# Kernel tuning notes

Hardware: AMD Instinct MI355X
Metric: run time of the kernel (lower is better)

## Reference

```python
import jax, jax.numpy as jnp
import numpy as np
from functools import partial

WARMUP = 365   # init kwarg warmup_length
HYDRODT = 1.0  # daily step

# (name, lower, upper) -- stands in for MODEL_PARAM_DICT['sac']['param_range']
PARAM_RANGES = [
    ("KC", 0.1, 1.2), ("PCTIM", 0.0, 0.1), ("ADIMP", 0.0, 0.3),
    ("UZTWM", 10.0, 100.0), ("UZFWM", 10.0, 100.0), ("LZTWM", 50.0, 400.0),
    ("LZFSM", 10.0, 100.0), ("LZFPM", 50.0, 1000.0), ("RSERV", 0.0, 0.3),
    ("PFREE", 0.0, 0.5), ("RIVA", 0.0, 0.1), ("ZPERC", 5.0, 350.0),
    ("REXP", 1.0, 4.0), ("UZK", 0.1, 0.5), ("LZSK", 0.01, 0.35),
    ("LZPK", 0.001, 0.05), ("CI", 0.5, 0.9), ("CGS", 0.95, 0.998),
    ("CGP", 0.98, 0.998), ("KE", 0.0, 1.0), ("XE", 0.0, 0.5),
]
_LO = np.array([r[1] for r in PARAM_RANGES], dtype=np.float32)
_HI = np.array([r[2] for r in PARAM_RANGES], dtype=np.float32)


def _scale_params(parameters):
    ps = _LO + parameters * (_HI - _LO)  # (n_basin, 21)
    return {name: ps[:, i] for i, (name, _, _) in enumerate(PARAM_RANGES)}


def _sac_step(prm, carry, pe_t):
    (auztw, alztw, uztw, uzfw, lztw, lzfs, lzfp, qs, qi, qgs, qgp, mq) = carry
    kc, pctim, adimp = prm["KC"], prm["PCTIM"], prm["ADIMP"]
    uztwm, uzfwm, lztwm = prm["UZTWM"], prm["UZFWM"], prm["LZTWM"]
    lzfsm, lzfpm = prm["LZFSM"], prm["LZFPM"]
    pfree, riva = prm["PFREE"], prm["RIVA"]
    zperc, rexp, uzk = prm["ZPERC"], prm["REXP"], prm["UZK"]
    lzsk, lzpk = prm["LZSK"], prm["LZPK"]
    ci, cgs, cgp, ke, xe = prm["CI"], prm["CGS"], prm["CGP"], prm["KE"], prm["XE"]

    p = jnp.maximum(pe_t[:, 0], 0.0)
    e = jnp.maximum(jnp.nan_to_num(pe_t[:, 1], nan=0.0, posinf=0.0, neginf=0.0), 0.0)
    ep = kc * e
    # --- impervious / alterable-impervious area ---
    roimp = pctim * p
    ae2 = pctim * ep
    ae1 = jnp.minimum(auztw, ep * (auztw / uztwm))
    ae3 = jnp.maximum((ep - ae1) * (alztw / (uztwm + lztwm)), 0.0)
    pav = jnp.maximum(p - (uztwm - (auztw - ae1)), 0.0)
    adsur = jnp.maximum(pav * ((alztw - ae3) / lztwm), 0.0)
    ars = jnp.maximum(pav - adsur + (alztw - ae3) - lztwm, 0.0)
    auztw = jnp.maximum(jnp.minimum(uztwm, auztw - ae1 + p), 0.0)
    alztw = jnp.maximum(jnp.minimum(lztwm, pav - adsur + (alztw - ae3)), 0.0)
    # --- permeable-area evaporation ---
    e1 = jnp.minimum(uztw, ep * (uztw / uztwm))
    e2 = jnp.maximum(jnp.minimum(uzfw, ep - e1), 0.0)
    e3 = jnp.maximum((ep - e1 - e2) * (lztw / (uztwm + lztwm)), 0.0)
    lt1 = jnp.maximum(lztw - e3, 0.0)
    e4 = riva * ep
    et = ae2 + ae1 + ae3 + e1 + e2 + e3 + e4
    adsur_adimp = adsur * adimp
    ars_adimp = ars * adimp
    parea = 1.0 - pctim - adimp
    # --- permeable-area runoff ---
    rs = jnp.maximum(p + (uztw + uzfw - e1 - e2) - (uztwm + uzfwm), 0.0) * parea
    ut = jnp.maximum(jnp.minimum(uztwm, uztw - e1 + p), 0.0)
    uf = jnp.maximum(jnp.minimum(uzfwm, p + (uztw + uzfw - e1 - e2) - ut), 0.0)
    ri = uf * uzk
    uf = jnp.maximum(uf - ri, 0.0)
    # --- percolation into the lower zone ---
    pbase = lzfsm * lzsk + lzfpm * lzpk
    defr = jnp.maximum(1.0 - (lzfs + lzfp + lt1) / (lzfsm + lzfpm + lztwm), 0.0)
    perc = pbase * (1.0 + zperc * jnp.power(defr, rexp)) * uf / uzfwm
    rate = jnp.maximum(jnp.minimum(perc, (lzfsm + lzfpm + lztwm) - (lzfs + lzfp + lt1)), 0.0)
    uf = jnp.maximum(uf - rate, 0.0)
    fx = jnp.maximum(jnp.minimum(lzfsm + lzfpm - (lzfs + lzfp),
                                 jnp.maximum(rate - (lztwm - lt1), rate * pfree)), 0.0)
    perct = rate - fx
    coef = (lzfpm / (lzfsm + lzfpm)) * (2.0 * (1.0 - lzfp / lzfpm)
           / ((1.0 - lzfp / lzfpm) + (1.0 - lzfs / lzfsm)))
    coef = jnp.minimum(coef, 1.0)
    percp = jnp.maximum(jnp.minimum(lzfpm - lzfp,
                                    jnp.maximum(fx - (lzfsm - lzfs), coef * fx)), 0.0)
    percs = jnp.maximum(fx - percp, 0.0)
    lt = jnp.minimum(lt1 + perct, lztwm)
    ls = lzfs + percs
    lp = lzfp + percp
    rgs = ls * lzsk
    ls = jnp.maximum(ls - rgs, 0.0)
    rgp = lp * lzpk
    lp = jnp.maximum(lp - rgp, 0.0)
    # --- area-weighted runoff components ---
    ri_p, rgs_p, rgp_p = ri * parea, rgs * parea, rgp * parea
    rs_tot = roimp + adsur_adimp + ars_adimp + rs
    # --- slope routing: linear reservoirs ---
    i1 = qs + qi + qgs + qgp  # previous-step total channel inflow
    qs_n = rs_tot
    qi_n = ci * qi + (1.0 - ci) * ri_p
    qgs_n = cgs * qgs + (1.0 - cgs) * rgs_p
    qgp_n = cgp * qgp + (1.0 - cgp) * rgp_p
    i2 = qs_n + qi_n + qgs_n + qgp_n
    # --- river routing: Muskingum, single reach (rivernumber = 1) ---
    dt = 0.5 * HYDRODT
    denom = ke * (1.0 - xe) + dt
    c1 = (ke * xe + dt) / denom
    c2 = (dt - ke * xe) / denom
    c3 = (ke * (1.0 - xe) - dt) / denom
    o1 = mq[:, 0]
    o2 = c1 * i1 + c2 * i2 + c3 * o1
    mq_n = o2[:, None]
    carry_n = (auztw, alztw, ut, uf, lt, ls, lp, qs_n, qi_n, qgs_n, qgp_n, mq_n)
    return carry_n, (et, o2)


def _sac_run(p_and_e, parameters, step_wrap=lambda f: f):
    prm = _scale_params(parameters)
    n_basin = parameters.shape[0]
    s01 = jnp.full((n_basin,), 0.01, dtype=p_and_e.dtype)
    carry = tuple(s01 for _ in range(11)) + (jnp.full((n_basin, 1), 0.01, dtype=p_and_e.dtype),)
    step = step_wrap(partial(_sac_step, prm))
    if WARMUP > 0:
        carry, _ = jax.lax.scan(step, carry, p_and_e[:WARMUP])
        carry = jax.tree_util.tree_map(jax.lax.stop_gradient, carry)  # torch no_grad warmup
    _, (e_sim, q_sim) = jax.lax.scan(step, carry, p_and_e[WARMUP:])
    return jnp.stack([q_sim, e_sim])  # (2, n_step, n_basin)


def setup_inputs() -> dict:
    key = jax.random.key(0)
    k1, k2, k3 = jax.random.split(key, 3)
    T, B = 1825, 10000
    prcp = jax.random.uniform(k1, (T, B), minval=0.0, maxval=20.0)  # mm/day
    pet = jax.random.uniform(k3, (T, B), minval=0.0, maxval=6.0)    # mm/day
    p_and_e = jnp.stack([prcp, pet], axis=-1).astype(jnp.float32)
    parameters = jax.random.uniform(k2, (B, 21), minval=0.01, maxval=0.99).astype(jnp.float32)
    return {"p_and_e": p_and_e, "parameters": parameters}


def reference(p_and_e, parameters):
    return _sac_run(p_and_e, parameters)
```

## Files before the change

kernel.cpp:

```cpp
#include <hip/hip_runtime.h>
#include <math.h>

#define T_TOTAL 1825
#define WARMUP_T 365
#define T_OUT (T_TOTAL - WARMUP_T)
#define NB 10000

__global__ __launch_bounds__(64, 1)
void sac_kernel(const float* __restrict__ p_and_e,
                const float* __restrict__ params,
                float* __restrict__ out)
{
    const int b = blockIdx.x * blockDim.x + threadIdx.x;
    if (b >= NB) return;

    const float* pr = params + b * 21;
    const float kc    = 0.1f   + pr[0]  * (1.2f - 0.1f);
    const float pctim = 0.0f   + pr[1]  * (0.1f - 0.0f);
    const float adimp = 0.0f   + pr[2]  * (0.3f - 0.0f);
    const float uztwm = 10.0f  + pr[3]  * (100.0f - 10.0f);
    const float uzfwm = 10.0f  + pr[4]  * (100.0f - 10.0f);
    const float lztwm = 50.0f  + pr[5]  * (400.0f - 50.0f);
    const float lzfsm = 10.0f  + pr[6]  * (100.0f - 10.0f);
    const float lzfpm = 50.0f  + pr[7]  * (1000.0f - 50.0f);
    const float pfree = 0.0f   + pr[9]  * (0.5f - 0.0f);
    const float riva  = 0.0f   + pr[10] * (0.1f - 0.0f);
    const float zperc = 5.0f   + pr[11] * (350.0f - 5.0f);
    const float rexp  = 1.0f   + pr[12] * (4.0f - 1.0f);
    const float uzk   = 0.1f   + pr[13] * (0.5f - 0.1f);
    const float lzsk  = 0.01f  + pr[14] * (0.35f - 0.01f);
    const float lzpk  = 0.001f + pr[15] * (0.05f - 0.001f);
    const float ci    = 0.5f   + pr[16] * (0.9f - 0.5f);
    const float cgs   = 0.95f  + pr[17] * (0.998f - 0.95f);
    const float cgp   = 0.98f  + pr[18] * (0.998f - 0.98f);
    const float ke    = 0.0f   + pr[19] * (1.0f - 0.0f);
    const float xe    = 0.0f   + pr[20] * (0.5f - 0.0f);

    const float inv_uztwm = 1.0f / uztwm;
    const float inv_lztwm = 1.0f / lztwm;
    const float inv_uzfwm = 1.0f / uzfwm;
    const float inv_uzlz  = 1.0f / (uztwm + lztwm);
    const float uz_sum    = uztwm + uzfwm;
    const float lzall     = lzfsm + lzfpm + lztwm;
    const float inv_lzall = 1.0f / lzall;
    const float lzfsfp    = lzfsm + lzfpm;
    const float ratio_fp  = lzfpm / lzfsfp;
    const float inv_lzfpm = 1.0f / lzfpm;
    const float inv_lzfsm = 1.0f / lzfsm;
    const float pbase     = lzfsm * lzsk + lzfpm * lzpk;
    const float parea     = 1.0f - pctim - adimp;
    const float one_m_ci  = 1.0f - ci;
    const float one_m_cgs = 1.0f - cgs;
    const float one_m_cgp = 1.0f - cgp;
    const float dt    = 0.5f;
    const float denom = ke * (1.0f - xe) + dt;
    const float c1 = (ke * xe + dt) / denom;
    const float c2 = (dt - ke * xe) / denom;
    const float c3 = (ke * (1.0f - xe) - dt) / denom;

    float auztw = 0.01f, alztw = 0.01f;
    float uztw = 0.01f, uzfw = 0.01f, lztw = 0.01f;
    float lzfs = 0.01f, lzfp = 0.01f;
    float qs = 0.01f, qi = 0.01f, qgs = 0.01f, qgp = 0.01f;
    float o_prev = 0.01f;

    const float2* __restrict__ pe2 = (const float2*)p_and_e;
    float* __restrict__ q_out = out;
    float* __restrict__ e_out = out + (size_t)T_OUT * NB;

    unsigned lidx = (unsigned)b;
    unsigned sidx = (unsigned)b;

    auto step = [&](float2 pe, bool do_store) {
        const float p = fmaxf(pe.x, 0.0f);
        const float e = fmaxf(pe.y, 0.0f);

        const float ep    = kc * e;

        const float ae1   = fminf(auztw, ep * (auztw * inv_uztwm));
        const float ae3   = fmaxf((ep - ae1) * (alztw * inv_uzlz), 0.0f);
        const float pav   = fmaxf(p - (uztwm - (auztw - ae1)), 0.0f);
        const float alz3  = alztw - ae3;
        const float adsur = fmaxf(pav * (alz3 * inv_lztwm), 0.0f);
        const float ars   = fmaxf(pav - adsur + alz3 - lztwm, 0.0f);
        const float auztw_n = fmaxf(fminf(uztwm, auztw - ae1 + p), 0.0f);
        const float alztw_n = fmaxf(fminf(lztwm, pav - adsur + alz3), 0.0f);

        const float gp = 1.0f - lzfp * inv_lzfpm;
        const float gs = 1.0f - lzfs * inv_lzfsm;
        float coef = ratio_fp * (2.0f * gp) * __builtin_amdgcn_rcpf(gp + gs);
        coef = fminf(coef, 1.0f);

        const float e1  = fminf(uztw, ep * (uztw * inv_uztwm));
        const float e2  = fmaxf(fminf(uzfw, ep - e1), 0.0f);
        const float e3  = fmaxf((ep - e1 - e2) * (lztw * inv_uzlz), 0.0f);
        const float lt1 = fmaxf(lztw - e3, 0.0f);

        const float uz_avail = p + (uztw + uzfw - e1 - e2);
        const float rs = fmaxf(uz_avail - uz_sum, 0.0f) * parea;
        const float ut = fmaxf(fminf(uztwm, uztw - e1 + p), 0.0f);
        float uf = fmaxf(fminf(uzfwm, uz_avail - ut), 0.0f);
        const float ri = uf * uzk;
        uf = fmaxf(uf - ri, 0.0f);

        const float lzsum = lzfs + lzfp + lt1;
        const float defr  = fmaxf(1.0f - lzsum * inv_lzall, 0.0f);
        const float dpow  = __builtin_amdgcn_exp2f(rexp * __builtin_amdgcn_logf(defr));
        const float perc  = pbase * (1.0f + zperc * dpow) * uf * inv_uzfwm;
        const float rate  = fmaxf(fminf(perc, lzall - lzsum), 0.0f);
        uf = fmaxf(uf - rate, 0.0f);

        const float fx = fmaxf(fminf(lzfsfp - (lzfs + lzfp),
                                     fmaxf(rate - (lztwm - lt1), rate * pfree)),
                               0.0f);
        const float perct = rate - fx;
        const float percp = fmaxf(fminf(lzfpm - lzfp,
                                        fmaxf(fx - (lzfsm - lzfs), coef * fx)),
                                  0.0f);
        const float percs = fmaxf(fx - percp, 0.0f);

        const float lt = fminf(lt1 + perct, lztwm);
        float ls = lzfs + percs;
        float lp = lzfp + percp;
        const float rgs = ls * lzsk;
        ls = fmaxf(ls - rgs, 0.0f);
        const float rgp = lp * lzpk;
        lp = fmaxf(lp - rgp, 0.0f);

        const float ri_p   = ri * parea;
        const float rgs_p  = rgs * parea;
        const float rgp_p  = rgp * parea;
        const float rs_tot = (pctim * p + adsur * adimp) + (ars * adimp + rs);

        const float i1 = (qs + qi) + (qgs + qgp);
        qs  = rs_tot;
        qi  = ci  * qi  + one_m_ci  * ri_p;
        qgs = cgs * qgs + one_m_cgs * rgs_p;
        qgp = cgp * qgp + one_m_cgp * rgp_p;
        const float i2 = (qs + qi) + (qgs + qgp);
        const float o2 = c1 * i1 + c2 * i2 + c3 * o_prev;
        o_prev = o2;

        if (do_store) {
            const float ae2 = pctim * ep;
            const float e4  = riva * ep;
            const float et  = (ae2 + ae1) + (ae3 + e1) + (e2 + e3) + e4;
            q_out[sidx] = o2;
            e_out[sidx] = et;
            sidx += NB;
        }

        auztw = auztw_n; alztw = alztw_n;
        uztw = ut; uzfw = uf; lztw = lt; lzfs = ls; lzfp = lp;
    };

    float2 f0 = pe2[lidx];
    float2 f1 = pe2[lidx + 1u * NB];
    float2 f2 = pe2[lidx + 2u * NB];
    float2 f3 = pe2[lidx + 3u * NB];
    lidx += 4u * NB;

    for (int g = 0; g < 91; ++g) {
        const float2 n0 = pe2[lidx];
        const float2 n1 = pe2[lidx + 1u * NB];
        const float2 n2 = pe2[lidx + 2u * NB];
        const float2 n3 = pe2[lidx + 3u * NB];
        lidx += 4u * NB;
        step(f0, false); step(f1, false); step(f2, false); step(f3, false);
        f0 = n0; f1 = n1; f2 = n2; f3 = n3;
    }
    {
        const float2 n0 = pe2[lidx];
        lidx += NB;
        step(f0, false);
        f0 = f1; f1 = f2; f2 = f3; f3 = n0;
    }

    for (int g = 0; g < 364; ++g) {
        const float2 n0 = pe2[lidx];
        const float2 n1 = pe2[lidx + 1u * NB];
        const float2 n2 = pe2[lidx + 2u * NB];
        const float2 n3 = pe2[lidx + 3u * NB];
        lidx += 4u * NB;
        step(f0, true); step(f1, true); step(f2, true); step(f3, true);
        f0 = n0; f1 = n1; f2 = n2; f3 = n3;
    }
    step(f0, true); step(f1, true); step(f2, true); step(f3, true);
}

extern "C" void kernel_launch(void* const* d_in, const int* in_sizes, int n_in,
                              void* d_out, int out_size, void* d_ws, size_t ws_size,
                              hipStream_t stream) {
    const float* p_and_e = (const float*)d_in[0];
    const float* params  = (const float*)d_in[1];
    float* out = (float*)d_out;

    const int block = 64;
    const int grid = (NB + block - 1) / block;
    sac_kernel<<<grid, block, 0, stream>>>(p_and_e, params, out);
}
```

Measured before the change: 681.1 us.

## Process two basins per thread with paired arithmetic and vectorized loads/stores

Each thread now simulates two adjacent basins using a paired-float struct, halving the thread count. Input loads become float4 and output stores float2. The aim is to interleave two independent dependency chains for ILP and enable packed FP32 math, and to widen memory accesses. The risk is that per-thread work doubles while occupancy halves, so total latency may rise if the chains were not bubble-bound.

```diff
diff --git a/kernel.cpp b/kernel.cpp
--- a/kernel.cpp
+++ b/kernel.cpp
@@ -5,183 +5,211 @@
 #define WARMUP_T 365
 #define T_OUT (T_TOTAL - WARMUP_T)
 #define NB 10000
+#define NPAIR 5000
+
+#define DI __device__ __forceinline__
+
+struct F2 { float a, b; };
+
+DI F2 operator+(F2 x, F2 y){ return {x.a + y.a, x.b + y.b}; }
+DI F2 operator-(F2 x, F2 y){ return {x.a - y.a, x.b - y.b}; }
+DI F2 operator*(F2 x, F2 y){ return {x.a * y.a, x.b * y.b}; }
+DI F2 operator+(float x, F2 y){ return {x + y.a, x + y.b}; }
+DI F2 operator-(float x, F2 y){ return {x - y.a, x - y.b}; }
+DI F2 operator*(float x, F2 y){ return {x * y.a, x * y.b}; }
+DI F2 vmin(F2 x, F2 y){ return {fminf(x.a, y.a), fminf(x.b, y.b)}; }
+DI F2 vmin(F2 x, float y){ return {fminf(x.a, y), fminf(x.b, y)}; }
+DI F2 vmax(F2 x, F2 y){ return {fmaxf(x.a, y.a), fmaxf(x.b, y.b)}; }
+DI F2 vmax(F2 x, float y){ return {fmaxf(x.a, y), fmaxf(x.b, y)}; }
+DI F2 clamp0(F2 x, F2 hi){
+    return {__builtin_amdgcn_fmed3f(x.a, 0.0f, hi.a),
+            __builtin_amdgcn_fmed3f(x.b, 0.0f, hi.b)};
+}
+DI F2 vrcp(F2 x){ return {__builtin_amdgcn_rcpf(x.a), __builtin_amdgcn_rcpf(x.b)}; }
+DI F2 vlog2(F2 x){ return {__builtin_amdgcn_logf(x.a), __builtin_amdgcn_logf(x.b)}; }
+DI F2 vexp2(F2 x){ return {__builtin_amdgcn_exp2f(x.a), __builtin_amdgcn_exp2f(x.b)}; }
+DI F2 vinv(F2 x){ return {1.0f / x.a, 1.0f / x.b}; }
+DI F2 vdiv(F2 x, F2 y){ return {x.a / y.a, x.b / y.b}; }
 
 __global__ __launch_bounds__(64, 1)
 void sac_kernel(const float* __restrict__ p_and_e,
                 const float* __restrict__ params,
                 float* __restrict__ out)
 {
-    const int b = blockIdx.x * blockDim.x + threadIdx.x;
-    if (b >= NB) return;
-
-    const float* pr = params + b * 21;
-    const float kc    = 0.1f   + pr[0]  * (1.2f - 0.1f);
-    const float pctim = 0.0f   + pr[1]  * (0.1f - 0.0f);
-    const float adimp = 0.0f   + pr[2]  * (0.3f - 0.0f);
-    const float uztwm = 10.0f  + pr[3]  * (100.0f - 10.0f);
-    const float uzfwm = 10.0f  + pr[4]  * (100.0f - 10.0f);
-    const float lztwm = 50.0f  + pr[5]  * (400.0f - 50.0f);
-    const float lzfsm = 10.0f  + pr[6]  * (100.0f - 10.0f);
-    const float lzfpm = 50.0f  + pr[7]  * (1000.0f - 50.0f);
-    const float pfree = 0.0f   + pr[9]  * (0.5f - 0.0f);
-    const float riva  = 0.0f   + pr[10] * (0.1f - 0.0f);
-    const float zperc = 5.0f   + pr[11] * (350.0f - 5.0f);
-    const float rexp  = 1.0f   + pr[12] * (4.0f - 1.0f);
-    const float uzk   = 0.1f   + pr[13] * (0.5f - 0.1f);
-    const float lzsk  = 0.01f  + pr[14] * (0.35f - 0.01f);
-    const float lzpk  = 0.001f + pr[15] * (0.05f - 0.001f);
-    const float ci    = 0.5f   + pr[16] * (0.9f - 0.5f);
-    const float cgs   = 0.95f  + pr[17] * (0.998f - 0.95f);
-    const float cgp   = 0.98f  + pr[18] * (0.998f - 0.98f);
-    const float ke    = 0.0f   + pr[19] * (1.0f - 0.0f);
-    const float xe    = 0.0f   + pr[20] * (0.5f - 0.0f);
-
-    const float inv_uztwm = 1.0f / uztwm;
-    const float inv_lztwm = 1.0f / lztwm;
-    const float inv_uzfwm = 1.0f / uzfwm;
-    const float inv_uzlz  = 1.0f / (uztwm + lztwm);
-    const float uz_sum    = uztwm + uzfwm;
-    const float lzall     = lzfsm + lzfpm + lztwm;
-    const float inv_lzall = 1.0f / lzall;
-    const float lzfsfp    = lzfsm + lzfpm;
-    const float ratio_fp  = lzfpm / lzfsfp;
-    const float inv_lzfpm = 1.0f / lzfpm;
-    const float inv_lzfsm = 1.0f / lzfsm;
-    const float pbase     = lzfsm * lzsk + lzfpm * lzpk;
-    const float parea     = 1.0f - pctim - adimp;
-    const float one_m_ci  = 1.0f - ci;
-    const float one_m_cgs = 1.0f - cgs;
-    const float one_m_cgp = 1.0f - cgp;
-    const float dt    = 0.5f;
-    const float denom = ke * (1.0f - xe) + dt;
-    const float c1 = (ke * xe + dt) / denom;
-    const float c2 = (dt - ke * xe) / denom;
-    const float c3 = (ke * (1.0f - xe) - dt) / denom;
-
-    float auztw = 0.01f, alztw = 0.01f;
-    float uztw = 0.01f, uzfw = 0.01f, lztw = 0.01f;
-    float lzfs = 0.01f, lzfp = 0.01f;
-    float qs = 0.01f, qi = 0.01f, qgs = 0.01f, qgp = 0.01f;
-    float o_prev = 0.01f;
-
-    const float2* __restrict__ pe2 = (const float2*)p_and_e;
-    float* __restrict__ q_out = out;
-    float* __restrict__ e_out = out + (size_t)T_OUT * NB;
-
-    unsigned lidx = (unsigned)b;
-    unsigned sidx = (unsigned)b;
-
-    auto step = [&](float2 pe, bool do_store) {
-        const float p = fmaxf(pe.x, 0.0f);
-        const float e = fmaxf(pe.y, 0.0f);
-
-        const float ep    = kc * e;
-
-        const float ae1   = fminf(auztw, ep * (auztw * inv_uztwm));
-        const float ae3   = fmaxf((ep - ae1) * (alztw * inv_uzlz), 0.0f);
-        const float pav   = fmaxf(p - (uztwm - (auztw - ae1)), 0.0f);
-        const float alz3  = alztw - ae3;
-        const float adsur = fmaxf(pav * (alz3 * inv_lztwm), 0.0f);
-        const float ars   = fmaxf(pav - adsur + alz3 - lztwm, 0.0f);
-        const float auztw_n = fmaxf(fminf(uztwm, auztw - ae1 + p), 0.0f);
-        const float alztw_n = fmaxf(fminf(lztwm, pav - adsur + alz3), 0.0f);
-
-        const float gp = 1.0f - lzfp * inv_lzfpm;
-        const float gs = 1.0f - lzfs * inv_lzfsm;
-        float coef = ratio_fp * (2.0f * gp) * __builtin_amdgcn_rcpf(gp + gs);
-        coef = fminf(coef, 1.0f);
-
-        const float e1  = fminf(uztw, ep * (uztw * inv_uztwm));
-        const float e2  = fmaxf(fminf(uzfw, ep - e1), 0.0f);
-        const float e3  = fmaxf((ep - e1 - e2) * (lztw * inv_uzlz), 0.0f);
-        const float lt1 = fmaxf(lztw - e3, 0.0f);
-
-        const float uz_avail = p + (uztw + uzfw - e1 - e2);
-        const float rs = fmaxf(uz_avail - uz_sum, 0.0f) * parea;
-        const float ut = fmaxf(fminf(uztwm, uztw - e1 + p), 0.0f);
-        float uf = fmaxf(fminf(uzfwm, uz_avail - ut), 0.0f);
-        const float ri = uf * uzk;
-        uf = fmaxf(uf - ri, 0.0f);
-
-        const float lzsum = lzfs + lzfp + lt1;
-        const float defr  = fmaxf(1.0f - lzsum * inv_lzall, 0.0f);
-        const float dpow  = __builtin_amdgcn_exp2f(rexp * __builtin_amdgcn_logf(defr));
-        const float perc  = pbase * (1.0f + zperc * dpow) * uf * inv_uzfwm;
-        const float rate  = fmaxf(fminf(perc, lzall - lzsum), 0.0f);
-        uf = fmaxf(uf - rate, 0.0f);
-
-        const float fx = fmaxf(fminf(lzfsfp - (lzfs + lzfp),
-                                     fmaxf(rate - (lztwm - lt1), rate * pfree)),
-                               0.0f);
-        const float perct = rate - fx;
-        const float percp = fmaxf(fminf(lzfpm - lzfp,
-                                        fmaxf(fx - (lzfsm - lzfs), coef * fx)),
-                                  0.0f);
-        const float percs = fmaxf(fx - percp, 0.0f);
-
-        const float lt = fminf(lt1 + perct, lztwm);
-        float ls = lzfs + percs;
-        float lp = lzfp + percp;
-        const float rgs = ls * lzsk;
-        ls = fmaxf(ls - rgs, 0.0f);
-        const float rgp = lp * lzpk;
-        lp = fmaxf(lp - rgp, 0.0f);
-
-        const float ri_p   = ri * parea;
-        const float rgs_p  = rgs * parea;
-        const float rgp_p  = rgp * parea;
-        const float rs_tot = (pctim * p + adsur * adimp) + (ars * adimp + rs);
-
-        const float i1 = (qs + qi) + (qgs + qgp);
+    const int i = blockIdx.x * blockDim.x + threadIdx.x;
+    if (i >= NPAIR) return;
+
+    const float* pr0 = params + (size_t)(2 * i) * 21;
+    const float* pr1 = pr0 + 21;
+#define LDP(k, lo, hi) F2{ (lo) + pr0[k] * ((hi) - (lo)), \
+                           (lo) + pr1[k] * ((hi) - (lo)) }
+    const F2 kc    = LDP(0,  0.1f,   1.2f);
+    const F2 pctim = LDP(1,  0.0f,   0.1f);
+    const F2 adimp = LDP(2,  0.0f,   0.3f);
+    const F2 uztwm = LDP(3,  10.0f,  100.0f);
+    const F2 uzfwm = LDP(4,  10.0f,  100.0f);
+    const F2 lztwm = LDP(5,  50.0f,  400.0f);
+    const F2 lzfsm = LDP(6,  10.0f,  100.0f);
+    const F2 lzfpm = LDP(7,  50.0f,  1000.0f);
+    const F2 pfree = LDP(9,  0.0f,   0.5f);
+    const F2 riva  = LDP(10, 0.0f,   0.1f);
+    const F2 zperc = LDP(11, 5.0f,   350.0f);
+    const F2 rexp  = LDP(12, 1.0f,   4.0f);
+    const F2 uzk   = LDP(13, 0.1f,   0.5f);
+    const F2 lzsk  = LDP(14, 0.01f,  0.35f);
+    const F2 lzpk  = LDP(15, 0.001f, 0.05f);
+    const F2 ci    = LDP(16, 0.5f,   0.9f);
+    const F2 cgs   = LDP(17, 0.95f,  0.998f);
+    const F2 cgp   = LDP(18, 0.98f,  0.998f);
+    const F2 ke    = LDP(19, 0.0f,   1.0f);
+    const F2 xe    = LDP(20, 0.0f,   0.5f);
+#undef LDP
+
+    const F2 inv_uztwm = vinv(uztwm);
+    const F2 inv_lztwm = vinv(lztwm);
+    const F2 inv_uzfwm = vinv(uzfwm);
+    const F2 inv_uzlz  = vinv(uztwm + lztwm);
+    const F2 uz_sum    = uztwm + uzfwm;
+    const F2 lzall     = lzfsm + lzfpm + lztwm;
+    const F2 inv_lzall = vinv(lzall);
+    const F2 lzfsfp    = lzfsm + lzfpm;
+    const F2 ratio_fp  = vdiv(lzfpm, lzfsfp);
+    const F2 inv_lzfpm = vinv(lzfpm);
+    const F2 inv_lzfsm = vinv(lzfsm);
+    const F2 pbase     = lzfsm * lzsk + lzfpm * lzpk;
+    const F2 parea     = 1.0f - pctim - adimp;
+    const F2 one_m_ci  = 1.0f - ci;
+    const F2 one_m_cgs = 1.0f - cgs;
+    const F2 one_m_cgp = 1.0f - cgp;
+    const float dt = 0.5f;
+    const F2 denom = ke * (1.0f - xe) + F2{dt, dt};
+    const F2 c1 = vdiv(ke * xe + F2{dt, dt}, denom);
+    const F2 c2 = vdiv(dt - ke * xe, denom);
+    const F2 c3 = vdiv(ke * (1.0f - xe) - F2{dt, dt}, denom);
+
+    F2 auztw = {0.01f, 0.01f}, alztw = {0.01f, 0.01f};
+    F2 uztw = {0.01f, 0.01f}, uzfw = {0.01f, 0.01f}, lztw = {0.01f, 0.01f};
+    F2 lzfs = {0.01f, 0.01f}, lzfp = {0.01f, 0.01f};
+    F2 qs = {0.01f, 0.01f}, qi = {0.01f, 0.01f};
+    F2 qgs = {0.01f, 0.01f}, qgp = {0.01f, 0.01f};
+    F2 o_prev = {0.01f, 0.01f};
+
+    const float4* __restrict__ pe4 = (const float4*)p_and_e;
+    float2* __restrict__ q2  = (float2*)out;
+    float2* __restrict__ e2o = (float2*)(out + (size_t)T_OUT * NB);
+
+    unsigned lidx = (unsigned)i;
+    unsigned sidx = (unsigned)i;
+
+    auto step = [&](float4 pe, bool do_store) {
+        const F2 p = vmax(F2{pe.x, pe.z}, 0.0f);
+        const F2 e = vmax(F2{pe.y, pe.w}, 0.0f);
+
+        const F2 ep = kc * e;
+
+        const F2 ae1   = vmin(auztw, ep * (auztw * inv_uztwm));
+        const F2 ae3   = vmax((ep - ae1) * (alztw * inv_uzlz), 0.0f);
+        const F2 pav   = vmax(p - (uztwm - (auztw - ae1)), 0.0f);
+        const F2 alz3  = alztw - ae3;
+        const F2 adsur = vmax(pav * (alz3 * inv_lztwm), 0.0f);
+        const F2 ars   = vmax(pav - adsur + alz3 - lztwm, 0.0f);
+        const F2 auztw_n = clamp0(auztw - ae1 + p, uztwm);
+        const F2 alztw_n = clamp0(pav - adsur + alz3, lztwm);
+
+        const F2 gp = 1.0f - lzfp * inv_lzfpm;
+        const F2 gs = 1.0f - lzfs * inv_lzfsm;
+        F2 coef = ratio_fp * (2.0f * gp) * vrcp(gp + gs);
+        coef = vmin(coef, 1.0f);
+
+        const F2 e1  = vmin(uztw, ep * (uztw * inv_uztwm));
+        const F2 e2v = clamp0(ep - e1, uzfw);
+        const F2 e3  = vmax((ep - e1 - e2v) * (lztw * inv_uzlz), 0.0f);
+        const F2 lt1 = vmax(lztw - e3, 0.0f);
+
+        const F2 uz_avail = p + (uztw + uzfw - e1 - e2v);
+        const F2 rs = vmax(uz_avail - uz_sum, 0.0f) * parea;
+        const F2 ut = clamp0(uztw - e1 + p, uztwm);
+        F2 uf = clamp0(uz_avail - ut, uzfwm);
+        const F2 ri = uf * uzk;
+        uf = vmax(uf - ri, 0.0f);
+
+        const F2 lzsum = lzfs + lzfp + lt1;
+        const F2 defr  = vmax(1.0f - lzsum * inv_lzall, 0.0f);
+        const F2 dpow  = vexp2(rexp * vlog2(defr));
+        const F2 perc  = pbase * (1.0f + zperc * dpow) * uf * inv_uzfwm;
+        const F2 rate  = clamp0(perc, lzall - lzsum);
+        uf = vmax(uf - rate, 0.0f);
+
+        const F2 fx = clamp0(vmax(rate - (lztwm - lt1), rate * pfree),
+                             lzfsfp - (lzfs + lzfp));
+        const F2 perct = rate - fx;
+        const F2 percp = clamp0(vmax(fx - (lzfsm - lzfs), coef * fx),
+                                lzfpm - lzfp);
+        const F2 percs = vmax(fx - percp, 0.0f);
+
+        const F2 lt = vmin(lt1 + perct, lztwm);
+        F2 ls = lzfs + percs;
+        F2 lp = lzfp + percp;
+        const F2 rgs = ls * lzsk;
+        ls = vmax(ls - rgs, 0.0f);
+        const F2 rgp = lp * lzpk;
+        lp = vmax(lp - rgp, 0.0f);
+
+        const F2 ri_p   = ri * parea;
+        const F2 rgs_p  = rgs * parea;
+        const F2 rgp_p  = rgp * parea;
+        const F2 rs_tot = (pctim * p + adsur * adimp) + (ars * adimp + rs);
+
+        const F2 i1 = (qs + qi) + (qgs + qgp);
         qs  = rs_tot;
         qi  = ci  * qi  + one_m_ci  * ri_p;
         qgs = cgs * qgs + one_m_cgs * rgs_p;
         qgp = cgp * qgp + one_m_cgp * rgp_p;
-        const float i2 = (qs + qi) + (qgs + qgp);
-        const float o2 = c1 * i1 + c2 * i2 + c3 * o_prev;
+        const F2 i2 = (qs + qi) + (qgs + qgp);
+        const F2 o2 = c1 * i1 + c2 * i2 + c3 * o_prev;
         o_prev = o2;
 
         if (do_store) {
-            const float ae2 = pctim * ep;
-            const float e4  = riva * ep;
-            const float et  = (ae2 + ae1) + (ae3 + e1) + (e2 + e3) + e4;
-            q_out[sidx] = o2;
-            e_out[sidx] = et;
-            sidx += NB;
+            const F2 ae2 = pctim * ep;
+            const F2 e4  = riva * ep;
+            const F2 et  = (ae2 + ae1) + (ae3 + e1) + (e2v + e3) + e4;
+            q2[sidx]  = make_float2(o2.a, o2.b);
+            e2o[sidx] = make_float2(et.a, et.b);
+            sidx += NPAIR;
         }
 
         auztw = auztw_n; alztw = alztw_n;
         uztw = ut; uzfw = uf; lztw = lt; lzfs = ls; lzfp = lp;
     };
 
-    float2 f0 = pe2[lidx];
-    float2 f1 = pe2[lidx + 1u * NB];
-    float2 f2 = pe2[lidx + 2u * NB];
-    float2 f3 = pe2[lidx + 3u * NB];
-    lidx += 4u * NB;
+    float4 f0 = pe4[lidx];
+    float4 f1 = pe4[lidx + 1u * NPAIR];
+    float4 f2 = pe4[lidx + 2u * NPAIR];
+    float4 f3 = pe4[lidx + 3u * NPAIR];
+    lidx += 4u * NPAIR;
 
     for (int g = 0; g < 91; ++g) {
-        const float2 n0 = pe2[lidx];
-        const float2 n1 = pe2[lidx + 1u * NB];
-        const float2 n2 = pe2[lidx + 2u * NB];
-        const float2 n3 = pe2[lidx + 3u * NB];
-        lidx += 4u * NB;
+        const float4 n0 = pe4[lidx];
+        const float4 n1 = pe4[lidx + 1u * NPAIR];
+        const float4 n2 = pe4[lidx + 2u * NPAIR];
+        const float4 n3 = pe4[lidx + 3u * NPAIR];
+        lidx += 4u * NPAIR;
         step(f0, false); step(f1, false); step(f2, false); step(f3, false);
         f0 = n0; f1 = n1; f2 = n2; f3 = n3;
     }
     {
-        const float2 n0 = pe2[lidx];
-        lidx += NB;
+        const float4 n0 = pe4[lidx];
+        lidx += NPAIR;
         step(f0, false);
         f0 = f1; f1 = f2; f2 = f3; f3 = n0;
     }
 
     for (int g = 0; g < 364; ++g) {
-        const float2 n0 = pe2[lidx];
-        const float2 n1 = pe2[lidx + 1u * NB];
-        const float2 n2 = pe2[lidx + 2u * NB];
-        const float2 n3 = pe2[lidx + 3u * NB];
-        lidx += 4u * NB;
+        const float4 n0 = pe4[lidx];
+        const float4 n1 = pe4[lidx + 1u * NPAIR];
+        const float4 n2 = pe4[lidx + 2u * NPAIR];
+        const float4 n3 = pe4[lidx + 3u * NPAIR];
+        lidx += 4u * NPAIR;
         step(f0, true); step(f1, true); step(f2, true); step(f3, true);
         f0 = n0; f1 = n1; f2 = n2; f3 = n3;
     }
@@ -196,6 +224,6 @@
     float* out = (float*)d_out;
 
     const int block = 64;
-    const int grid = (NB + block - 1) / block;
+    const int grid = (NPAIR + block - 1) / block;
     sac_kernel<<<grid, block, 0, stream>>>(p_and_e, params, out);
 }
```

Measured after the change: 944.4 us. +38.7%, slower.
